# Performance work log

Measured on AMD Instinct MI355X. Metric: run time of the kernel, lower is better.

## Reference

```python
import jax, jax.numpy as jnp
import numpy as np

COORD_DIM = 2
ENTITY_DIM = 1024
FIELD_DIM = 512
INPUT_DIM = 512
NUM_ENTITIES = 512
FIELD_RESOLUTION = 10000  # grid_size = 100


def _gelu(x):
    return jax.nn.gelu(x, approximate=False)  # torch nn.GELU default (erf)


def setup_inputs() -> dict:
    key = jax.random.key(0)
    ks = jax.random.split(key, 9)
    std = 0.02  # matches _init_parameters
    B, S = 8, 4096
    x = jax.random.normal(ks[0], (B, S, INPUT_DIM), dtype=jnp.float32)
    # DensityField: density_projection = Linear(D,F) GELU Linear(F,F) GELU; coordinate_generator = Linear(F,2)
    W1 = jax.random.normal(ks[1], (INPUT_DIM, FIELD_DIM), jnp.float32) * std
    b1 = jnp.zeros((FIELD_DIM,), jnp.float32)
    W2 = jax.random.normal(ks[2], (FIELD_DIM, FIELD_DIM), jnp.float32) * std
    b2 = jnp.zeros((FIELD_DIM,), jnp.float32)
    Wc = jax.random.normal(ks[3], (FIELD_DIM, COORD_DIM), jnp.float32) * std
    bc = jnp.zeros((COORD_DIM,), jnp.float32)
    # entity_mapper: Linear(F+2, F) GELU Linear(F, E+2+1)
    We1 = jax.random.normal(ks[4], (FIELD_DIM + COORD_DIM, FIELD_DIM), jnp.float32) * std
    be1 = jnp.zeros((FIELD_DIM,), jnp.float32)
    We2 = jax.random.normal(ks[5], (FIELD_DIM, ENTITY_DIM + COORD_DIM + 1), jnp.float32) * std
    be2 = jnp.zeros((ENTITY_DIM + COORD_DIM + 1,), jnp.float32)
    # output_projection: Linear(E, 2E) GELU Linear(2E, D)
    Wo1 = jax.random.normal(ks[6], (ENTITY_DIM, 2 * ENTITY_DIM), jnp.float32) * std
    bo1 = jnp.zeros((2 * ENTITY_DIM,), jnp.float32)
    Wo2 = jax.random.normal(ks[7], (2 * ENTITY_DIM, INPUT_DIM), jnp.float32) * std
    bo2 = jnp.zeros((INPUT_DIM,), jnp.float32)
    return dict(x=x, W1=W1, b1=b1, W2=W2, b2=b2, Wc=Wc, bc=bc,
                We1=We1, be1=be1, We2=We2, be2=be2,
                Wo1=Wo1, bo1=bo1, Wo2=Wo2, bo2=bo2)


def _forward(x, W1, b1, W2, b2, Wc, bc, We1, be1, We2, be2, Wo1, bo1, Wo2, bo2):
    # --- DensityField ---
    df = _gelu(_gelu(x @ W1 + b1) @ W2 + b2)          # [B,S,F]
    coords = df @ Wc + bc                              # [B,S,2]
    # --- ContinuousEntityExtractor ---
    field_input = jnp.concatenate([coords, df], axis=-1)          # [B,S,2+F]
    ef = _gelu(field_input @ We1 + be1) @ We2 + be2                # [B,S,E+3]
    importance = jnp.linalg.norm(ef, axis=-1)                      # [B,S]
    _, top_idx = jax.lax.top_k(importance, NUM_ENTITIES)           # [B,Ne]
    sel = jnp.take_along_axis(ef, top_idx[..., None], axis=1)     # [B,Ne,E+3]
    positions = sel[..., :COORD_DIM]                               # [B,Ne,2]
    states = sel[..., COORD_DIM:COORD_DIM + ENTITY_DIM]            # [B,Ne,E]
    # --- ContinuousOutputGenerator ---
    proj = _gelu(states @ Wo1 + bo1) @ Wo2 + bo2                   # [B,Ne,D]
    grid_size = int(FIELD_RESOLUTION ** 0.5)
    g = jnp.linspace(-1.0, 1.0, grid_size)
    gx, gy = jnp.meshgrid(g, g, indexing='ij')
    grid = jnp.stack([gx.ravel(), gy.ravel()], axis=-1)            # [G2,2]
    # squared euclidean distances via expansion (torch: cdist then **2)
    g2 = jnp.sum(grid * grid, axis=-1)                             # [G2]
    p2 = jnp.sum(positions * positions, axis=-1)                   # [B,Ne]
    gp = jnp.einsum('gc,bnc->bgn', grid, positions)                # [B,G2,Ne]
    sq = g2[None, :, None] + p2[:, None, :] - 2.0 * gp             # [B,G2,Ne]
    attn = jnp.exp(-sq / 0.1)
    attn = attn / (attn.sum(axis=-1, keepdims=True) + 1e-8)
    out = jnp.einsum('bgn,bnd->bgd', attn, proj)                   # [B,G2,D]
    return out


def reference(x, W1, b1, W2, b2, Wc, bc, We1, be1, We2, be2, Wo1, bo1, Wo2, bo2):
    return _forward(x, W1, b1, W2, b2, Wc, bc, We1, be1, We2, be2, Wo1, bo1, Wo2, bo2)
```

## Files before the change

kernel.cpp:

```cpp
#include <hip/hip_runtime.h>
#include <hip/hip_bf16.h>
#include <math.h>


typedef __attribute__((ext_vector_type(8))) short bf16x8;
typedef __attribute__((ext_vector_type(4))) float f32x4;

__device__ __forceinline__ float gelu_exact(float x) {
    return 0.5f * x * (1.0f + erff(x * 0.7071067811865476f));
}

__device__ __forceinline__ void async_copy16(const void* g, void* l) {
    __builtin_amdgcn_global_load_lds(
        (const __attribute__((address_space(1))) unsigned int*)g,
        (__attribute__((address_space(3))) unsigned int*)l, 16, 0, 0);
}

__global__ __launch_bounds__(256) void split_kernel(
    const float* __restrict__ in,
    __hip_bfloat16* __restrict__ hi, __hip_bfloat16* __restrict__ lo)
{
    const int i4 = blockIdx.x * 256 + threadIdx.x;
    const float4 v = ((const float4*)in)[i4];
    __hip_bfloat16 h0 = __float2bfloat16(v.x);
    __hip_bfloat16 h1 = __float2bfloat16(v.y);
    __hip_bfloat16 h2 = __float2bfloat16(v.z);
    __hip_bfloat16 h3 = __float2bfloat16(v.w);
    __hip_bfloat16 l0 = __float2bfloat16(v.x - __bfloat162float(h0));
    __hip_bfloat16 l1 = __float2bfloat16(v.y - __bfloat162float(h1));
    __hip_bfloat16 l2 = __float2bfloat16(v.z - __bfloat162float(h2));
    __hip_bfloat16 l3 = __float2bfloat16(v.w - __bfloat162float(h3));
    union { __hip_bfloat16 h[4]; short4 s; } uh, ul;
    uh.h[0] = h0; uh.h[1] = h1; uh.h[2] = h2; uh.h[3] = h3;
    ul.h[0] = l0; ul.h[1] = l1; ul.h[2] = l2; ul.h[3] = l3;
    ((short4*)hi)[i4] = uh.s;
    ((short4*)lo)[i4] = ul.s;
}

__global__ __launch_bounds__(256) void transpose_split_kernel(
    const float* __restrict__ in,
    __hip_bfloat16* __restrict__ outH, __hip_bfloat16* __restrict__ outL,
    int K, int N)
{
    __shared__ float tile[32][33];
    const int k0 = blockIdx.y * 32, n0 = blockIdx.x * 32;
    const int t = threadIdx.x;
    const int lr = t >> 5, lc = t & 31;
    #pragma unroll
    for (int p = 0; p < 4; p++) {
        const int r = p * 8 + lr;
        const int n = n0 + lc;
        tile[r][lc] = (n < N) ? in[(size_t)(k0 + r) * N + n] : 0.f;
    }
    __syncthreads();
    #pragma unroll
    for (int p = 0; p < 4; p++) {
        const int r = p * 8 + lr;
        const float v = tile[lc][r];
        const __hip_bfloat16 h = __float2bfloat16(v);
        const __hip_bfloat16 l = __float2bfloat16(v - __bfloat162float(h));
        outH[(size_t)(n0 + r) * K + k0 + lc] = h;
        outL[(size_t)(n0 + r) * K + k0 + lc] = l;
    }
}

template<bool GELU, bool RANK2, bool SPLIT, bool BOUNDS>
__device__ __forceinline__ void gemm3k_body(
    const __hip_bfloat16* __restrict__ Ahi, const __hip_bfloat16* __restrict__ Alo,
    const __hip_bfloat16* __restrict__ Bhi, const __hip_bfloat16* __restrict__ Blo,
    const float* __restrict__ bias,
    float* __restrict__ Cf, int ldc,
    __hip_bfloat16* __restrict__ Chi, __hip_bfloat16* __restrict__ Clo,
    int N,
    const float* __restrict__ A2, const float* __restrict__ W2r)
{
    __shared__ __align__(16) __hip_bfloat16 AsH[128][32];
    __shared__ __align__(16) __hip_bfloat16 AsL[128][32];
    __shared__ __align__(16) __hip_bfloat16 BsH[128][32];
    __shared__ __align__(16) __hip_bfloat16 BsL[128][32];
    const int t = threadIdx.x;
    const int wave = t >> 6, lane = t & 63;
    const int wave_m = wave >> 1, wave_n = wave & 1;
    const int fr = lane & 15, quad = lane >> 4;
    const int gx = gridDim.x;
    const int L = blockIdx.y * gx + blockIdx.x;
    const int xcd = L & 7, rem = L >> 3;
    const int mchunk = gridDim.y >> 3;
    const int m0 = (xcd * mchunk + rem / gx) * 128;
    const int n0 = (rem % gx) * 128;
    const int srow = lane >> 2;
    const int skc  = (lane & 3) * 8;

    f32x4 acc[4][4] = {};

    for (int k0 = 0; k0 < 512; k0 += 32) {
        #pragma unroll
        for (int s = 0; s < 2; s++) {
            const int seg = wave * 2 + s;
            const int row = seg * 16 + srow;
            const size_t ao = (size_t)(m0 + row) * 512 + k0 + skc;
            const size_t bo = (size_t)(n0 + row) * 512 + k0 + skc;
            async_copy16(Ahi + ao, &AsH[seg * 16][0]);
            async_copy16(Alo + ao, &AsL[seg * 16][0]);
            async_copy16(Bhi + bo, &BsH[seg * 16][0]);
            async_copy16(Blo + bo, &BsL[seg * 16][0]);
        }
        __syncthreads();
        bf16x8 ah[4], al[4], bh[4], bl[4];
        #pragma unroll
        for (int i = 0; i < 4; i++) {
            ah[i] = *(const bf16x8*)&AsH[wave_m * 64 + i * 16 + fr][quad * 8];
            al[i] = *(const bf16x8*)&AsL[wave_m * 64 + i * 16 + fr][quad * 8];
        }
        #pragma unroll
        for (int j = 0; j < 4; j++) {
            bh[j] = *(const bf16x8*)&BsH[wave_n * 64 + j * 16 + fr][quad * 8];
            bl[j] = *(const bf16x8*)&BsL[wave_n * 64 + j * 16 + fr][quad * 8];
        }
        #pragma unroll
        for (int i = 0; i < 4; i++)
            #pragma unroll
            for (int j = 0; j < 4; j++)
                acc[i][j] = __builtin_amdgcn_mfma_f32_16x16x32_bf16(
                    ah[i], bh[j], acc[i][j], 0, 0, 0);
        #pragma unroll
        for (int i = 0; i < 4; i++)
            #pragma unroll
            for (int j = 0; j < 4; j++)
                acc[i][j] = __builtin_amdgcn_mfma_f32_16x16x32_bf16(
                    ah[i], bl[j], acc[i][j], 0, 0, 0);
        #pragma unroll
        for (int i = 0; i < 4; i++)
            #pragma unroll
            for (int j = 0; j < 4; j++)
                acc[i][j] = __builtin_amdgcn_mfma_f32_16x16x32_bf16(
                    al[i], bh[j], acc[i][j], 0, 0, 0);
        __syncthreads();
    }

    #pragma unroll
    for (int i = 0; i < 4; i++) {
        const int gmb = m0 + wave_m * 64 + i * 16 + quad * 4;
        #pragma unroll
        for (int j = 0; j < 4; j++) {
            const int gn = n0 + wave_n * 64 + j * 16 + fr;
            const bool nok = !BOUNDS || (gn < N);
            const float bv = nok ? bias[gn] : 0.f;
            float w2a = 0.f, w2b = 0.f;
            if (RANK2) { w2a = W2r[gn]; w2b = W2r[512 + gn]; }
            #pragma unroll
            for (int r = 0; r < 4; r++) {
                const int gm = gmb + r;
                float v = acc[i][j][r] + bv;
                if (RANK2)
                    v += A2[(size_t)gm * 2] * w2a + A2[(size_t)gm * 2 + 1] * w2b;
                if (GELU) v = gelu_exact(v);
                if (SPLIT) {
                    const __hip_bfloat16 h = __float2bfloat16(v);
                    const __hip_bfloat16 l =
                        __float2bfloat16(v - __bfloat162float(h));
                    Chi[(size_t)gm * 512 + gn] = h;
                    Clo[(size_t)gm * 512 + gn] = l;
                } else if (nok) {
                    Cf[(size_t)gm * ldc + gn] = v;
                }
            }
        }
    }
}

__global__ __launch_bounds__(256) void gemm_h1(
    const __hip_bfloat16* __restrict__ Ahi, const __hip_bfloat16* __restrict__ Alo,
    const __hip_bfloat16* __restrict__ Bhi, const __hip_bfloat16* __restrict__ Blo,
    const float* __restrict__ bias,
    __hip_bfloat16* __restrict__ Chi, __hip_bfloat16* __restrict__ Clo)
{
    gemm3k_body<true, false, true, false>(
        Ahi, Alo, Bhi, Blo, bias, nullptr, 0, Chi, Clo, 512, nullptr, nullptr);
}

__global__ __launch_bounds__(256) void gemm_df(
    const __hip_bfloat16* __restrict__ Ahi, const __hip_bfloat16* __restrict__ Alo,
    const __hip_bfloat16* __restrict__ Bhi, const __hip_bfloat16* __restrict__ Blo,
    const float* __restrict__ bias,
    __hip_bfloat16* __restrict__ Chi, __hip_bfloat16* __restrict__ Clo)
{
    gemm3k_body<true, false, true, false>(
        Ahi, Alo, Bhi, Blo, bias, nullptr, 0, Chi, Clo, 512, nullptr, nullptr);
}

__global__ __launch_bounds__(256) void gemm_h3(
    const __hip_bfloat16* __restrict__ Ahi, const __hip_bfloat16* __restrict__ Alo,
    const __hip_bfloat16* __restrict__ Bhi, const __hip_bfloat16* __restrict__ Blo,
    const float* __restrict__ bias,
    __hip_bfloat16* __restrict__ Chi, __hip_bfloat16* __restrict__ Clo,
    const float* __restrict__ A2, const float* __restrict__ W2r)
{
    gemm3k_body<true, true, true, false>(
        Ahi, Alo, Bhi, Blo, bias, nullptr, 0, Chi, Clo, 512, A2, W2r);
}

__global__ __launch_bounds__(256) void gemm_ef(
    const __hip_bfloat16* __restrict__ Ahi, const __hip_bfloat16* __restrict__ Alo,
    const __hip_bfloat16* __restrict__ Bhi, const __hip_bfloat16* __restrict__ Blo,
    const float* __restrict__ bias,
    float* __restrict__ Cf)
{
    gemm3k_body<false, false, false, true>(
        Ahi, Alo, Bhi, Blo, bias, Cf, 1027, nullptr, nullptr, 1027,
        nullptr, nullptr);
}

__global__ __launch_bounds__(256) void coords_kernel(
    const __hip_bfloat16* __restrict__ DFh, const __hip_bfloat16* __restrict__ DFl,
    const float* __restrict__ Wc,
    const float* __restrict__ bc, float* __restrict__ CRD)
{
    const int gid  = blockIdx.x * 256 + threadIdx.x;
    const int row  = gid >> 6;
    const int lane = gid & 63;
    const __hip_bfloat16* dh = DFh + (size_t)row * 512;
    const __hip_bfloat16* dl = DFl + (size_t)row * 512;
    float s0 = 0.f, s1 = 0.f;
    for (int k = lane; k < 512; k += 64) {
        const float v = __bfloat162float(dh[k]) + __bfloat162float(dl[k]);
        const float2 wc = ((const float2*)Wc)[k];
        s0 += v * wc.x;
        s1 += v * wc.y;
    }
    #pragma unroll
    for (int off = 32; off; off >>= 1) {
        s0 += __shfl_down(s0, off);
        s1 += __shfl_down(s1, off);
    }
    if (lane == 0) {
        CRD[(size_t)row * 2 + 0] = s0 + bc[0];
        CRD[(size_t)row * 2 + 1] = s1 + bc[1];
    }
}

__global__ __launch_bounds__(256) void importance_kernel(
    const float* __restrict__ EF, float* __restrict__ IMP)
{
    const int gid  = blockIdx.x * 256 + threadIdx.x;
    const int row  = gid >> 6;
    const int lane = gid & 63;
    const float* e = EF + (size_t)row * 1027;
    float ss = 0.f;
    for (int k = lane; k < 1027; k += 64) { const float v = e[k]; ss += v * v; }
    #pragma unroll
    for (int off = 32; off; off >>= 1) ss += __shfl_down(ss, off);
    if (lane == 0) IMP[row] = sqrtf(ss);
}

__global__ __launch_bounds__(1024) void topk_kernel(
    const float* __restrict__ IMP, int* __restrict__ IDX)
{
    __shared__ float v[4096];
    __shared__ int   ix[4096];
    const int b = blockIdx.x, t = threadIdx.x;
    for (int i = t; i < 4096; i += 1024) { v[i] = IMP[b * 4096 + i]; ix[i] = i; }
    __syncthreads();
    for (int k = 2; k <= 4096; k <<= 1) {
        for (int j = k >> 1; j > 0; j >>= 1) {
            for (int q = 0; q < 4; q++) {
                const int i = t + (q << 10);
                const int l = i ^ j;
                if (l > i) {
                    const float vi = v[i], vl = v[l];
                    const int   ii = ix[i], il = ix[l];
                    const bool after = (vi < vl) || (vi == vl && ii > il);
                    const bool dirAsc = ((i & k) == 0);
                    if (dirAsc ? after : !after) {
                        v[i] = vl; v[l] = vi; ix[i] = il; ix[l] = ii;
                    }
                }
            }
            __syncthreads();
        }
    }
    if (t < 512) IDX[b * 512 + t] = ix[t];
}

__global__ __launch_bounds__(256) void gather_kernel(
    const float* __restrict__ EF, const int* __restrict__ IDX,
    float* __restrict__ POS, __hip_bfloat16* __restrict__ ST)
{
    const int bn  = blockIdx.x;
    const int b   = bn >> 9;
    const int row = IDX[bn];
    const float* src = EF + ((size_t)(b * 4096) + row) * 1027;
    const int t = threadIdx.x;
    if (t < 2) POS[(size_t)bn * 2 + t] = src[t];
    __hip_bfloat16* dst = ST + (size_t)bn * 1024;
    for (int k = t; k < 1024; k += 256) dst[k] = __float2bfloat16(src[2 + k]);
}

__global__ __launch_bounds__(256) void transpose_cvt_kernel(
    const float* __restrict__ in, __hip_bfloat16* __restrict__ out,
    int K, int N)
{
    __shared__ float tile[32][33];
    const int k0 = blockIdx.y * 32, n0 = blockIdx.x * 32;
    const int t = threadIdx.x;
    const int lr = t >> 5, lc = t & 31;
    #pragma unroll
    for (int p = 0; p < 4; p++) {
        const int r = p * 8 + lr;
        tile[r][lc] = in[(size_t)(k0 + r) * N + n0 + lc];
    }
    __syncthreads();
    #pragma unroll
    for (int p = 0; p < 4; p++) {
        const int r = p * 8 + lr;
        out[(size_t)(n0 + r) * K + k0 + lc] = __float2bfloat16(tile[lc][r]);
    }
}

__global__ __launch_bounds__(256) void transpose_proj_kernel(
    const __hip_bfloat16* __restrict__ in, __hip_bfloat16* __restrict__ out)
{
    __shared__ __hip_bfloat16 tile[32][33];
    const int b = blockIdx.z;
    const int n0 = blockIdx.y * 32, d0 = blockIdx.x * 32;
    const int t = threadIdx.x;
    const int lr = t >> 5, lc = t & 31;
    #pragma unroll
    for (int p = 0; p < 4; p++) {
        const int r = p * 8 + lr;
        tile[r][lc] = in[((size_t)b * 512 + n0 + r) * 512 + d0 + lc];
    }
    __syncthreads();
    #pragma unroll
    for (int p = 0; p < 4; p++) {
        const int r = p * 8 + lr;
        out[((size_t)b * 512 + d0 + r) * 512 + n0 + lc] = tile[lc][r];
    }
}

template<bool GELU>
__device__ __forceinline__ void gemm_post_body(
    const __hip_bfloat16* __restrict__ A,
    const __hip_bfloat16* __restrict__ BT,
    const float* __restrict__ bias,
    __hip_bfloat16* __restrict__ C,
    int N, int K)
{
    __shared__ __align__(16) __hip_bfloat16 As[2][128][32];
    __shared__ __align__(16) __hip_bfloat16 Bs[2][128][32];
    const int t = threadIdx.x;
    const int wave = t >> 6, lane = t & 63;
    const int wave_m = wave >> 1, wave_n = wave & 1;
    const int fr = lane & 15, quad = lane >> 4;
    const int gx = gridDim.x;
    const int nwg = gx * gridDim.y;
    int lid = blockIdx.y * gx + blockIdx.x;
    {
        const int chunk = nwg >> 3;
        lid = (lid & 7) * chunk + (lid >> 3);
    }
    const int m0 = (lid / gx) * 128;
    const int n0 = (lid % gx) * 128;
    const int srow = lane >> 2;
    const int skc  = (lane & 3) * 8;
    const int nsteps = K >> 5;

    f32x4 acc[4][4] = {};

    auto STAGE = [&](int buf, int step) {
        const int kk = step << 5;
        #pragma unroll
        for (int s = 0; s < 2; s++) {
            const int seg = wave * 2 + s;
            const int row = seg * 16 + srow;
            async_copy16(A  + (size_t)(m0 + row) * K + kk + skc,
                         &As[buf][seg * 16][0]);
            async_copy16(BT + (size_t)(n0 + row) * K + kk + skc,
                         &Bs[buf][seg * 16][0]);
        }
    };

    STAGE(0, 0);
    __syncthreads();
    int cur = 0;
    for (int step = 0; step < nsteps; ++step) {
        if (step + 1 < nsteps) STAGE(cur ^ 1, step + 1);
        bf16x8 af[4], bfv[4];
        #pragma unroll
        for (int i = 0; i < 4; i++)
            af[i] = *(const bf16x8*)&As[cur][wave_m * 64 + i * 16 + fr][quad * 8];
        #pragma unroll
        for (int j = 0; j < 4; j++)
            bfv[j] = *(const bf16x8*)&Bs[cur][wave_n * 64 + j * 16 + fr][quad * 8];
        #pragma unroll
        for (int i = 0; i < 4; i++)
            #pragma unroll
            for (int j = 0; j < 4; j++)
                acc[i][j] = __builtin_amdgcn_mfma_f32_16x16x32_bf16(
                    af[i], bfv[j], acc[i][j], 0, 0, 0);
        __syncthreads();
        cur ^= 1;
    }
    #pragma unroll
    for (int i = 0; i < 4; i++) {
        const int gm = m0 + wave_m * 64 + i * 16 + quad * 4;
        #pragma unroll
        for (int j = 0; j < 4; j++) {
            const int gn = n0 + wave_n * 64 + j * 16 + fr;
            const float bv = bias[gn];
            #pragma unroll
            for (int r = 0; r < 4; r++) {
                float v = acc[i][j][r] + bv;
                if (GELU) v = gelu_exact(v);
                C[(size_t)(gm + r) * N + gn] = __float2bfloat16(v);
            }
        }
    }
}

__global__ __launch_bounds__(256, 4) void gemm_o1(
    const __hip_bfloat16* __restrict__ A, const __hip_bfloat16* __restrict__ BT,
    const float* __restrict__ bias, __hip_bfloat16* __restrict__ C,
    int N, int K)
{
    gemm_post_body<true>(A, BT, bias, C, N, K);
}

__global__ __launch_bounds__(256, 4) void gemm_o2(
    const __hip_bfloat16* __restrict__ A, const __hip_bfloat16* __restrict__ BT,
    const float* __restrict__ bias, __hip_bfloat16* __restrict__ C,
    int N, int K)
{
    gemm_post_body<false>(A, BT, bias, C, N, K);
}

__global__ __launch_bounds__(256) void attn_mfma_kernel(
    const float* __restrict__ POS,
    const __hip_bfloat16* __restrict__ PROJT,
    float* __restrict__ OUT)
{
    __shared__ __align__(16) __hip_bfloat16 Bs[256][32];
    __shared__ float2 pos_s[512];
    __shared__ float srow_s[4][16];
    const int t = threadIdx.x;
    const int wave = t >> 6, lane = t & 63;
    const int fr = lane & 15, quad = lane >> 4;
    const int b  = blockIdx.z;
    const int g0 = blockIdx.x * 64;
    const int d0 = blockIdx.y * 256;

    {
        const float2* p = (const float2*)(POS + (size_t)b * 512 * 2);
        pos_s[t]       = p[t];
        pos_s[256 + t] = p[256 + t];
    }
    const int g = g0 + wave * 16 + fr;
    const bool gv = g < 10000;
    const float step = 2.0f / 99.0f;
    const int gi = gv ? (g / 100) : 0;
    const int gj = gv ? (g - gi * 100) : 0;
    const float gx = -1.f + step * (float)gi;
    const float gy = -1.f + step * (float)gj;

    f32x4 acc[16] = {};
    float wsum = 0.f;
    __syncthreads();

    for (int n0 = 0; n0 < 512; n0 += 32) {
        #pragma unroll
        for (int s = 0; s < 4; s++) {
            const int seg = wave * 4 + s;
            const __hip_bfloat16* gB = PROJT
                + ((size_t)b * 512 + d0 + seg * 16 + (lane >> 2)) * 512
                + n0 + (lane & 3) * 8;
            async_copy16(gB, &Bs[seg * 16][0]);
        }
        bf16x8 wf;
        float wl = 0.f;
        #pragma unroll
        for (int j = 0; j < 8; j++) {
            const int n = n0 + quad * 8 + j;
            const float2 pn = pos_s[n];
            const float dx = gx - pn.x, dy = gy - pn.y;
            const float w = gv ? __expf(-10.0f * (dx * dx + dy * dy)) : 0.f;
            const __hip_bfloat16 wb = __float2bfloat16(w);
            union { __hip_bfloat16 h; short s; } u; u.h = wb;
            wf[j] = u.s;
            wl += __bfloat162float(wb);
        }
        wsum += wl;
        __syncthreads();
        #pragma unroll
        for (int j = 0; j < 16; j++) {
            const bf16x8 bv = *(const bf16x8*)&Bs[j * 16 + fr][quad * 8];
            acc[j] = __builtin_amdgcn_mfma_f32_16x16x32_bf16(wf, bv, acc[j], 0, 0, 0);
        }
        __syncthreads();
    }
    wsum += __shfl_xor(wsum, 16);
    wsum += __shfl_xor(wsum, 32);
    if (lane < 16) srow_s[wave][lane] = wsum;
    __syncthreads();
    const int rbase = quad * 4;
    float inv[4];
    #pragma unroll
    for (int r = 0; r < 4; r++)
        inv[r] = 1.0f / (srow_s[wave][rbase + r] + 1e-8f);
    #pragma unroll
    for (int j = 0; j < 16; j++) {
        const int col = d0 + j * 16 + fr;
        #pragma unroll
        for (int r = 0; r < 4; r++) {
            const int gr = g0 + wave * 16 + rbase + r;
            if (gr < 10000)
                OUT[((size_t)b * 10000 + gr) * 512 + col] = acc[j][r] * inv[r];
        }
    }
}

extern "C" void kernel_launch(void* const* d_in, const int* in_sizes, int n_in,
                              void* d_out, int out_size, void* d_ws, size_t ws_size,
                              hipStream_t stream)
{
    const float* x   = (const float*)d_in[0];
    const float* W1  = (const float*)d_in[1];
    const float* b1  = (const float*)d_in[2];
    const float* W2  = (const float*)d_in[3];
    const float* b2  = (const float*)d_in[4];
    const float* Wc  = (const float*)d_in[5];
    const float* bc  = (const float*)d_in[6];
    const float* We1 = (const float*)d_in[7];
    const float* be1 = (const float*)d_in[8];
    const float* We2 = (const float*)d_in[9];
    const float* be2 = (const float*)d_in[10];
    const float* Wo1 = (const float*)d_in[11];
    const float* bo1 = (const float*)d_in[12];
    const float* Wo2 = (const float*)d_in[13];
    const float* bo2 = (const float*)d_in[14];
    float* out = (float*)d_out;

    const size_t BS = 32768;
    const size_t ACT = BS * 512;
    __hip_bfloat16* P0h = (__hip_bfloat16*)d_ws;
    __hip_bfloat16* P0l = P0h + ACT;
    __hip_bfloat16* P1h = P0l + ACT;
    __hip_bfloat16* P1l = P1h + ACT;
    float* EF  = (float*)(P1l + ACT);
    float* CRD = EF + BS * 1027;
    float* IMP = CRD + BS * 2;
    int*   IDX = (int*)(IMP + BS);
    float* POS = (float*)(IDX + 4096);
    __hip_bfloat16* W1Th = (__hip_bfloat16*)(POS + 4096 * 2);
    __hip_bfloat16* W1Tl = W1Th + 512 * 512;
    __hip_bfloat16* W2Th = W1Tl + 512 * 512;
    __hip_bfloat16* W2Tl = W2Th + 512 * 512;
    __hip_bfloat16* We1Th = W2Tl + 512 * 512;
    __hip_bfloat16* We1Tl = We1Th + 512 * 512;
    __hip_bfloat16* We2Th = We1Tl + 512 * 512;
    __hip_bfloat16* We2Tl = We2Th + (size_t)1152 * 512;
    __hip_bfloat16* ST    = P0h;
    __hip_bfloat16* H4    = ST + (size_t)4096 * 1024;
    __hip_bfloat16* PROJ  = H4 + (size_t)4096 * 2048;
    __hip_bfloat16* PROJT = PROJ + (size_t)4096 * 512;
    __hip_bfloat16* Wo1T  = PROJT + (size_t)4096 * 512;
    __hip_bfloat16* Wo2T  = Wo1T + (size_t)2048 * 1024;

    dim3 blk(256);
    split_kernel<<<dim3(16384), blk, 0, stream>>>(x, P0h, P0l);
    transpose_split_kernel<<<dim3(16, 16), blk, 0, stream>>>(W1, W1Th, W1Tl, 512, 512);
    transpose_split_kernel<<<dim3(16, 16), blk, 0, stream>>>(W2, W2Th, W2Tl, 512, 512);
    transpose_split_kernel<<<dim3(16, 16), blk, 0, stream>>>(We1 + 2 * 512, We1Th, We1Tl, 512, 512);
    transpose_split_kernel<<<dim3(36, 16), blk, 0, stream>>>(We2, We2Th, We2Tl, 512, 1027);
    gemm_h1<<<dim3(4, 256), blk, 0, stream>>>(
        P0h, P0l, W1Th, W1Tl, b1, P1h, P1l);
    gemm_df<<<dim3(4, 256), blk, 0, stream>>>(
        P1h, P1l, W2Th, W2Tl, b2, P0h, P0l);
    coords_kernel<<<dim3(8192), blk, 0, stream>>>(P0h, P0l, Wc, bc, CRD);
    gemm_h3<<<dim3(4, 256), blk, 0, stream>>>(
        P0h, P0l, We1Th, We1Tl, be1, P1h, P1l, CRD, We1);
    gemm_ef<<<dim3(9, 256), blk, 0, stream>>>(
        P1h, P1l, We2Th, We2Tl, be2, EF);
    importance_kernel<<<dim3(8192), blk, 0, stream>>>(EF, IMP);
    topk_kernel<<<dim3(8), dim3(1024), 0, stream>>>(IMP, IDX);
    transpose_cvt_kernel<<<dim3(64, 32), blk, 0, stream>>>(Wo1, Wo1T, 1024, 2048);
    transpose_cvt_kernel<<<dim3(16, 64), blk, 0, stream>>>(Wo2, Wo2T, 2048, 512);
    gather_kernel<<<dim3(4096), blk, 0, stream>>>(EF, IDX, POS, ST);
    gemm_o1<<<dim3(16, 32), blk, 0, stream>>>(ST, Wo1T, bo1, H4, 2048, 1024);
    gemm_o2<<<dim3(4, 32), blk, 0, stream>>>(H4, Wo2T, bo2, PROJ, 512, 2048);
    transpose_proj_kernel<<<dim3(16, 16, 8), blk, 0, stream>>>(PROJ, PROJT);
    attn_mfma_kernel<<<dim3(157, 2, 8), blk, 0, stream>>>(POS, PROJT, out);
}
```

Measured before the change: 899.3 us.

## Double-buffer split-bf16 GEMM LDS tiles with async prefetch two steps ahead

Turns the single-buffered LDS staging in the shared 3-pass bf16 GEMM body into a two-stage ring. Global-to-LDS loads for step k+2 are issued while step k's MFMAs run, using explicit vmcnt waits and raw barriers. The LDS layout changes to a chunk-major order (16 rows by 8 elements per quad) to cut bank conflicts on the fragment reads. It also raises MFMA issue priority and sets launch_bounds(256,2). The cost is twice the LDS (64KB), which may limit occupancy, and correctness now depends on the hand-written waitcnt and barrier ordering.

```diff
diff --git a/kernel.cpp b/kernel.cpp
--- a/kernel.cpp
+++ b/kernel.cpp
@@ -74,10 +74,10 @@
     int N,
     const float* __restrict__ A2, const float* __restrict__ W2r)
 {
-    __shared__ __align__(16) __hip_bfloat16 AsH[128][32];
-    __shared__ __align__(16) __hip_bfloat16 AsL[128][32];
-    __shared__ __align__(16) __hip_bfloat16 BsH[128][32];
-    __shared__ __align__(16) __hip_bfloat16 BsL[128][32];
+    __shared__ __align__(16) __hip_bfloat16 AsH[2][4096];
+    __shared__ __align__(16) __hip_bfloat16 AsL[2][4096];
+    __shared__ __align__(16) __hip_bfloat16 BsH[2][4096];
+    __shared__ __align__(16) __hip_bfloat16 BsL[2][4096];
     const int t = threadIdx.x;
     const int wave = t >> 6, lane = t & 63;
     const int wave_m = wave >> 1, wave_n = wave & 1;
@@ -88,35 +88,52 @@
     const int mchunk = gridDim.y >> 3;
     const int m0 = (xcd * mchunk + rem / gx) * 128;
     const int n0 = (rem % gx) * 128;
-    const int srow = lane >> 2;
-    const int skc  = (lane & 3) * 8;
+    const int lrow   = lane & 15;
+    const int lchunk = (lane >> 4) * 8;
 
     f32x4 acc[4][4] = {};
 
-    for (int k0 = 0; k0 < 512; k0 += 32) {
+    auto STAGE = [&](int buf, int step) {
+        const int kk = step << 5;
         #pragma unroll
         for (int s = 0; s < 2; s++) {
             const int seg = wave * 2 + s;
-            const int row = seg * 16 + srow;
-            const size_t ao = (size_t)(m0 + row) * 512 + k0 + skc;
-            const size_t bo = (size_t)(n0 + row) * 512 + k0 + skc;
-            async_copy16(Ahi + ao, &AsH[seg * 16][0]);
-            async_copy16(Alo + ao, &AsL[seg * 16][0]);
-            async_copy16(Bhi + bo, &BsH[seg * 16][0]);
-            async_copy16(Blo + bo, &BsL[seg * 16][0]);
-        }
-        __syncthreads();
+            const size_t ao = (size_t)(m0 + seg * 16 + lrow) * 512 + kk + lchunk;
+            const size_t bo = (size_t)(n0 + seg * 16 + lrow) * 512 + kk + lchunk;
+            async_copy16(Ahi + ao, &AsH[buf][seg * 512]);
+            async_copy16(Alo + ao, &AsL[buf][seg * 512]);
+            async_copy16(Bhi + bo, &BsH[buf][seg * 512]);
+            async_copy16(Blo + bo, &BsL[buf][seg * 512]);
+        }
+    };
+
+    const int abase = wave_m * 2048 + quad * 128 + fr * 8;
+    const int bbase = wave_n * 2048 + quad * 128 + fr * 8;
+
+    STAGE(0, 0);
+    STAGE(1, 1);
+
+    for (int step = 0; step < 16; ++step) {
+        if (step < 15) asm volatile("s_waitcnt vmcnt(8)" ::: "memory");
+        else           asm volatile("s_waitcnt vmcnt(0)" ::: "memory");
+        __builtin_amdgcn_s_barrier();
+        const int buf = step & 1;
         bf16x8 ah[4], al[4], bh[4], bl[4];
         #pragma unroll
         for (int i = 0; i < 4; i++) {
-            ah[i] = *(const bf16x8*)&AsH[wave_m * 64 + i * 16 + fr][quad * 8];
-            al[i] = *(const bf16x8*)&AsL[wave_m * 64 + i * 16 + fr][quad * 8];
+            ah[i] = *(const bf16x8*)&AsH[buf][abase + i * 512];
+            al[i] = *(const bf16x8*)&AsL[buf][abase + i * 512];
         }
         #pragma unroll
         for (int j = 0; j < 4; j++) {
-            bh[j] = *(const bf16x8*)&BsH[wave_n * 64 + j * 16 + fr][quad * 8];
-            bl[j] = *(const bf16x8*)&BsL[wave_n * 64 + j * 16 + fr][quad * 8];
-        }
+            bh[j] = *(const bf16x8*)&BsH[buf][bbase + j * 512];
+            bl[j] = *(const bf16x8*)&BsL[buf][bbase + j * 512];
+        }
+        asm volatile("s_waitcnt lgkmcnt(0)" ::: "memory");
+        __builtin_amdgcn_sched_barrier(0);
+        __builtin_amdgcn_s_barrier();
+        if (step + 2 < 16) STAGE(buf, step + 2);
+        __builtin_amdgcn_s_setprio(1);
         #pragma unroll
         for (int i = 0; i < 4; i++)
             #pragma unroll
@@ -135,7 +152,7 @@
             for (int j = 0; j < 4; j++)
                 acc[i][j] = __builtin_amdgcn_mfma_f32_16x16x32_bf16(
                     al[i], bh[j], acc[i][j], 0, 0, 0);
-        __syncthreads();
+        __builtin_amdgcn_s_setprio(0);
     }
 
     #pragma unroll
@@ -169,7 +186,7 @@
     }
 }
 
-__global__ __launch_bounds__(256) void gemm_h1(
+__global__ __launch_bounds__(256, 2) void gemm_h1(
     const __hip_bfloat16* __restrict__ Ahi, const __hip_bfloat16* __restrict__ Alo,
     const __hip_bfloat16* __restrict__ Bhi, const __hip_bfloat16* __restrict__ Blo,
     const float* __restrict__ bias,
@@ -179,7 +196,7 @@
         Ahi, Alo, Bhi, Blo, bias, nullptr, 0, Chi, Clo, 512, nullptr, nullptr);
 }
 
-__global__ __launch_bounds__(256) void gemm_df(
+__global__ __launch_bounds__(256, 2) void gemm_df(
     const __hip_bfloat16* __restrict__ Ahi, const __hip_bfloat16* __restrict__ Alo,
     const __hip_bfloat16* __restrict__ Bhi, const __hip_bfloat16* __restrict__ Blo,
     const float* __restrict__ bias,
@@ -189,7 +206,7 @@
         Ahi, Alo, Bhi, Blo, bias, nullptr, 0, Chi, Clo, 512, nullptr, nullptr);
 }
 
-__global__ __launch_bounds__(256) void gemm_h3(
+__global__ __launch_bounds__(256, 2) void gemm_h3(
     const __hip_bfloat16* __restrict__ Ahi, const __hip_bfloat16* __restrict__ Alo,
     const __hip_bfloat16* __restrict__ Bhi, const __hip_bfloat16* __restrict__ Blo,
     const float* __restrict__ bias,
@@ -200,7 +217,7 @@
         Ahi, Alo, Bhi, Blo, bias, nullptr, 0, Chi, Clo, 512, A2, W2r);
 }
 
-__global__ __launch_bounds__(256) void gemm_ef(
+__global__ __launch_bounds__(256, 2) void gemm_ef(
     const __hip_bfloat16* __restrict__ Ahi, const __hip_bfloat16* __restrict__ Alo,
     const __hip_bfloat16* __restrict__ Bhi, const __hip_bfloat16* __restrict__ Blo,
     const float* __restrict__ bias,
```

Result: slower. 949.6 us (+5.6%).
